# Kernel tuning notes

Hardware: AMD Instinct MI355X
Metric: run time of the kernel (lower is better)

## Reference

```python
import jax, jax.numpy as jnp
import numpy as np

# BCQLinear packed forward: weight[o, i] reconstructed from per-(out,group,bit)
# alpha scales and +/-1 binary codes via einsum('oib,oiab->oia'), then a plain
# out-channel-wise matmul (in_ch_wise=False) plus bias. beta is NOT used in the
# packed forward path of the original module.

B, S = 2, 1024          # token dims (m...)
O = 4096                 # out_features
G, A, NB = 32, 128, 3    # n_groups, group_size, n_bits; in_features = G*A = 4096


def setup_inputs() -> dict:
    key = jax.random.key(0)
    k1, k2, k3, k4 = jax.random.split(key, 4)
    x = jax.random.normal(k1, (B, S, G * A), dtype=jnp.float32)
    # binary codes are strictly +/-1 (Packer.unpack yields sign bits)
    b = jnp.sign(jax.random.normal(k2, (O, G, A, NB)))
    binary = jnp.where(b == 0, 1.0, b).astype(jnp.float32)
    # alpha scales are small positive magnitudes in practice
    alpha = jax.random.uniform(k3, (O, G, NB), dtype=jnp.float32,
                               minval=0.01, maxval=0.1)
    bias = 0.01 * jax.random.normal(k4, (O,), dtype=jnp.float32)
    return {"input": x, "binary": binary, "alpha": alpha, "bias": bias}


def reference(input, binary, alpha, bias):
    # dequantize: [O, G, A] -> [O, I]
    weight = jnp.einsum('oib,oiab->oia', alpha, binary).reshape(binary.shape[0], -1)
    # out-channel-wise matmul: m...i, oi -> m...o
    out = jnp.einsum('msi,oi->mso', input, weight) + bias
    return out
```

## Files before the change

### kernel.cpp

```cpp
#include <hip/hip_runtime.h>
#include <hip/hip_bf16.h>
#include <stdint.h>

typedef __bf16 bf16x8 __attribute__((ext_vector_type(8)));
typedef float  f32x4  __attribute__((ext_vector_type(4)));

static constexpr int Mdim = 2048;
static constexpr int Ndim = 4096;
static constexpr int Kdim = 4096;
static constexpr int DQ_BLOCKS = (Ndim * Kdim / 8) / 256;
static constexpr int CVT_BLOCKS = (Mdim * Kdim / 8) / 256;

__global__ __launch_bounds__(256)
void prep(const float* __restrict__ binary, const float* __restrict__ alpha,
          const float* __restrict__ x, __bf16* __restrict__ w,
          __bf16* __restrict__ xb) {
  const int b = blockIdx.x;
  if (b < DQ_BLOCKS) {
    long e = ((long)b * 256 + threadIdx.x) * 8;
    int o = (int)(e >> 12);
    int g = (int)((e & 4095) >> 7);
    const float* al = alpha + ((long)o * 32 + g) * 3;
    float a0 = al[0], a1 = al[1], a2 = al[2];
    const float4* q = (const float4*)(binary + e * 3);
    float4 q0 = q[0], q1 = q[1], q2 = q[2], q3 = q[3], q4 = q[4], q5 = q[5];
    bf16x8 wv;
    wv[0] = (__bf16)(a0 * q0.x + a1 * q0.y + a2 * q0.z);
    wv[1] = (__bf16)(a0 * q0.w + a1 * q1.x + a2 * q1.y);
    wv[2] = (__bf16)(a0 * q1.z + a1 * q1.w + a2 * q2.x);
    wv[3] = (__bf16)(a0 * q2.y + a1 * q2.z + a2 * q2.w);
    wv[4] = (__bf16)(a0 * q3.x + a1 * q3.y + a2 * q3.z);
    wv[5] = (__bf16)(a0 * q3.w + a1 * q4.x + a2 * q4.y);
    wv[6] = (__bf16)(a0 * q4.z + a1 * q4.w + a2 * q5.x);
    wv[7] = (__bf16)(a0 * q5.y + a1 * q5.z + a2 * q5.w);
    *(bf16x8*)(w + e) = wv;
  } else {
    long e = ((long)(b - DQ_BLOCKS) * 256 + threadIdx.x) * 8;
    float4 v0 = *(const float4*)(x + e);
    float4 v1 = *(const float4*)(x + e + 4);
    bf16x8 r;
    r[0] = (__bf16)v0.x; r[1] = (__bf16)v0.y; r[2] = (__bf16)v0.z; r[3] = (__bf16)v0.w;
    r[4] = (__bf16)v1.x; r[5] = (__bf16)v1.y; r[6] = (__bf16)v1.z; r[7] = (__bf16)v1.w;
    *(bf16x8*)(xb + e) = r;
  }
}

__global__ __launch_bounds__(256)
void reduce_add(const __bf16* __restrict__ p, const float* __restrict__ bias,
                float* __restrict__ out) {
  long e = ((long)blockIdx.x * 256 + threadIdx.x) * 8;
  bf16x8 a = *(const bf16x8*)(p + e);
  bf16x8 c = *(const bf16x8*)(p + (long)Mdim * Ndim + e);
  int col = (int)(e & (Ndim - 1));
  float4 bv0 = *(const float4*)(bias + col);
  float4 bv1 = *(const float4*)(bias + col + 4);
  float4 r0, r1;
  r0.x = (float)a[0] + (float)c[0] + bv0.x;
  r0.y = (float)a[1] + (float)c[1] + bv0.y;
  r0.z = (float)a[2] + (float)c[2] + bv0.z;
  r0.w = (float)a[3] + (float)c[3] + bv0.w;
  r1.x = (float)a[4] + (float)c[4] + bv1.x;
  r1.y = (float)a[5] + (float)c[5] + bv1.y;
  r1.z = (float)a[6] + (float)c[6] + bv1.z;
  r1.w = (float)a[7] + (float)c[7] + bv1.w;
  *(float4*)(out + e) = r0;
  *(float4*)(out + e + 4) = r1;
}

static constexpr int KSLICE = 2048;
static constexpr int NT = KSLICE / 64;
static constexpr int HB = 65536;

__device__ __forceinline__ void g2l16(const void* g, void* l) {
  __builtin_amdgcn_global_load_lds(
      (const __attribute__((address_space(1))) void*)g,
      (__attribute__((address_space(3))) void*)l, 16, 0, 0);
}

#define BAR()    __builtin_amdgcn_s_barrier()
#define LGKM0()  asm volatile("s_waitcnt lgkmcnt(0)" ::: "memory")
#define SCHED0() __builtin_amdgcn_sched_barrier(0)
#define GATE8()  asm volatile("s_waitcnt vmcnt(8)" ::: "memory")
#define GATE0()  asm volatile("s_waitcnt vmcnt(0)" ::: "memory")

#define STAGE_A1(t, bo) do { \
  g2l16(baseA +                 (long)(t) * 64, sm + (bo) +     0 + w * 1024); \
  g2l16(baseA + 128L * Kdim   + (long)(t) * 64, sm + (bo) + 16384 + w * 1024); \
} while (0)
#define STAGE_A2(t, bo) do { \
  g2l16(baseA +  64L * Kdim   + (long)(t) * 64, sm + (bo) +  8192 + w * 1024); \
  g2l16(baseA + 192L * Kdim   + (long)(t) * 64, sm + (bo) + 24576 + w * 1024); \
} while (0)
#define STAGE_B1(t, bo) do { \
  g2l16(baseB +                 (long)(t) * 64, sm + (bo) + 32768 + bq * 1024); \
  g2l16(baseB +   8L * Kdim   + (long)(t) * 64, sm + (bo) + 32768 + bq * 1024 + 1024); \
} while (0)
#define STAGE_B2(t, bo) do { \
  g2l16(baseB +  32L * Kdim   + (long)(t) * 64, sm + (bo) + 32768 + bq * 1024 + 4096); \
  g2l16(baseB +  40L * Kdim   + (long)(t) * 64, sm + (bo) + 32768 + bq * 1024 + 5120); \
} while (0)

#define LOAD_A4(dst, bo, m0_) do { \
  _Pragma("unroll") for (int m_ = 0; m_ < 4; ++m_) \
    _Pragma("unroll") for (int h_ = 0; h_ < 2; ++h_) \
      dst[m_][h_] = *(const bf16x8*)(sm + (bo) + aoffbase + ((m0_) + m_) * 2048 + swz[h_]); \
} while (0)
#define LOAD_B2(dst, bo, n0_) do { \
  _Pragma("unroll") for (int n_ = 0; n_ < 2; ++n_) \
    _Pragma("unroll") for (int h_ = 0; h_ < 2; ++h_) \
      dst[n_][h_] = *(const bf16x8*)(sm + (bo) + boffbase + ((n0_) + n_) * 2048 + swz[h_]); \
} while (0)

#define MMA8(fa_, fb_, m0_, n0_) do { \
  __builtin_amdgcn_s_setprio(1); \
  _Pragma("unroll") for (int m_ = 0; m_ < 4; ++m_) \
    _Pragma("unroll") for (int n_ = 0; n_ < 2; ++n_) { \
      acc[(m0_) + m_][(n0_) + n_] = __builtin_amdgcn_mfma_f32_16x16x32_bf16( \
          fa_[m_][0], fb_[n_][0], acc[(m0_) + m_][(n0_) + n_], 0, 0, 0); \
      acc[(m0_) + m_][(n0_) + n_] = __builtin_amdgcn_mfma_f32_16x16x32_bf16( \
          fa_[m_][1], fb_[n_][1], acc[(m0_) + m_][(n0_) + n_], 0, 0, 0); \
    } \
  __builtin_amdgcn_s_setprio(0); \
} while (0)

#define KTILE(t_, bo, PF_, LASTGATE) do { \
   \
  LOAD_A4(fa, bo, 0); LOAD_B2(fb01, bo, 0); \
  BAR(); LGKM0(); SCHED0(); \
  MMA8(fa, fb01, 0, 0); \
  BAR(); \
   \
  LOAD_B2(fb23, bo, 2); \
  if (PF_) { STAGE_A1((t_) + 2, bo); STAGE_B1((t_) + 2, bo); } \
  BAR(); LGKM0(); SCHED0(); \
  MMA8(fa, fb23, 0, 2); \
  BAR(); \
   \
  LOAD_A4(fa, bo, 4); \
  if (PF_) STAGE_B2((t_) + 2, bo); \
  BAR(); LGKM0(); SCHED0(); \
  MMA8(fa, fb01, 4, 0); \
  BAR(); \
   \
  if (PF_) { STAGE_A2((t_) + 2, bo); GATE8(); } else { LASTGATE; } \
  BAR(); \
  MMA8(fa, fb23, 4, 2); \
  BAR(); \
} while (0)

__global__ __launch_bounds__(512, 2)
void gemm256(const __bf16* __restrict__ A, const __bf16* __restrict__ Bw,
             __bf16* __restrict__ P) {
  __shared__ __align__(128) char sm[2 * HB];
  const int tid = threadIdx.x, lane = tid & 63, w = tid >> 6;
  const int wm = w >> 2, wn = w & 3;

  const int bid = blockIdx.x;
  const int logical = (bid & 7) * 32 + (bid >> 3);
  const int ks = logical >> 7;
  const int tile = logical & 127;
  const int tm = tile & 7, tn = tile >> 3;
  const int kbase = ks * KSLICE;

  __bf16* Pout = P + (long)ks * Mdim * Ndim;

  const int rlo = lane >> 3;
  const int gsw = (lane & 7) ^ rlo;
  const __bf16* baseA = A + (long)(tm * 256 + w * 8 + rlo) * Kdim + kbase + gsw * 8;
  const __bf16* baseB = Bw + (long)(tn * 256 + (w >> 1) * 64 + (w & 1) * 16 + rlo) * Kdim
                        + kbase + gsw * 8;
  const int bq = (w >> 1) * 8 + (w & 1) * 2;

  int swz[2];
#pragma unroll
  for (int h = 0; h < 2; ++h)
    swz[h] = (((h * 4 + (lane >> 4)) ^ (lane & 7)) << 4);
  const int aoffbase = (wm * 128 + (lane & 15)) * 128;
  const int boffbase = 32768 + (wn * 64 + (lane & 15)) * 128;

  f32x4 acc[8][4] = {};
  bf16x8 fa[4][2], fb01[2][2], fb23[2][2];

  STAGE_A1(0, 0);  STAGE_B1(0, 0);  STAGE_B2(0, 0);  STAGE_A2(0, 0);
  STAGE_A1(1, HB); STAGE_B1(1, HB); STAGE_B2(1, HB); STAGE_A2(1, HB);
  GATE8();
  BAR();

  for (int i = 0; i < NT / 2; ++i) {
    const int t0 = 2 * i, t1 = 2 * i + 1;
    const bool pf = (i < NT / 2 - 1);
    KTILE(t0, 0,  pf, GATE0());
    KTILE(t1, HB, pf, GATE0());
  }

  const int r4 = (lane >> 4) * 4;
  const int cl = lane & 15;
#pragma unroll
  for (int m = 0; m < 8; ++m)
#pragma unroll
    for (int n = 0; n < 4; ++n)
#pragma unroll
      for (int r = 0; r < 4; ++r) {
        int row = tm * 256 + wm * 128 + m * 16 + r4 + r;
        int col = tn * 256 + wn * 64 + n * 16 + cl;
        Pout[(long)row * Ndim + col] = (__bf16)acc[m][n][r];
      }
}

extern "C" void kernel_launch(void* const* d_in, const int* in_sizes, int n_in,
                              void* d_out, int out_size, void* d_ws, size_t ws_size,
                              hipStream_t stream) {
  const float* x      = (const float*)d_in[0];
  const float* binary = (const float*)d_in[1];
  const float* alpha  = (const float*)d_in[2];
  const float* bias   = (const float*)d_in[3];
  float* out = (float*)d_out;

  __bf16* wb = (__bf16*)d_ws;
  __bf16* xb = wb + (size_t)Ndim * Kdim;
  __bf16* pp = xb + (size_t)Mdim * Kdim;

  prep<<<dim3(DQ_BLOCKS + CVT_BLOCKS), 256, 0, stream>>>(binary, alpha, x, wb, xb);
  gemm256<<<dim3(256), 512, 0, stream>>>(xb, wb, pp);
  reduce_add<<<dim3(Mdim * Ndim / 8 / 256), 256, 0, stream>>>(pp, bias, out);
}
```

Before: 123.3 us.

## Fuse split-K reduction and bias into GEMM via per-tile atomic counters

Removes the separate reduce_add kernel. Each split-K block now writes its bf16 partial tile in a fragment-native layout and increments a per-tile atomic counter. The second block to arrive reads the other partial, adds it in registers, and writes the fp32 output plus bias through LDS so stores are coalesced. This saves a kernel launch and a full pass over the partial buffer, but adds atomics, cross-block memory-ordering requirements, and a serialized epilogue in the last-arriving block.

```diff
diff --git a/kernel.cpp b/kernel.cpp
--- a/kernel.cpp
+++ b/kernel.cpp
@@ -3,6 +3,7 @@
 #include <stdint.h>
 
 typedef __bf16 bf16x8 __attribute__((ext_vector_type(8)));
+typedef __bf16 bf16x4 __attribute__((ext_vector_type(4)));
 typedef float  f32x4  __attribute__((ext_vector_type(4)));
 
 static constexpr int Mdim = 2048;
@@ -14,10 +15,12 @@
 __global__ __launch_bounds__(256)
 void prep(const float* __restrict__ binary, const float* __restrict__ alpha,
           const float* __restrict__ x, __bf16* __restrict__ w,
-          __bf16* __restrict__ xb) {
+          __bf16* __restrict__ xb, int* __restrict__ flags) {
   const int b = blockIdx.x;
+  const int t = threadIdx.x;
+  if (b == 0 && t < 128) flags[t] = 0;
   if (b < DQ_BLOCKS) {
-    long e = ((long)b * 256 + threadIdx.x) * 8;
+    long e = ((long)b * 256 + t) * 8;
     int o = (int)(e >> 12);
     int g = (int)((e & 4095) >> 7);
     const float* al = alpha + ((long)o * 32 + g) * 3;
@@ -35,7 +38,7 @@
     wv[7] = (__bf16)(a0 * q5.y + a1 * q5.z + a2 * q5.w);
     *(bf16x8*)(w + e) = wv;
   } else {
-    long e = ((long)(b - DQ_BLOCKS) * 256 + threadIdx.x) * 8;
+    long e = ((long)(b - DQ_BLOCKS) * 256 + t) * 8;
     float4 v0 = *(const float4*)(x + e);
     float4 v1 = *(const float4*)(x + e + 4);
     bf16x8 r;
@@ -43,28 +46,6 @@
     r[4] = (__bf16)v1.x; r[5] = (__bf16)v1.y; r[6] = (__bf16)v1.z; r[7] = (__bf16)v1.w;
     *(bf16x8*)(xb + e) = r;
   }
-}
-
-__global__ __launch_bounds__(256)
-void reduce_add(const __bf16* __restrict__ p, const float* __restrict__ bias,
-                float* __restrict__ out) {
-  long e = ((long)blockIdx.x * 256 + threadIdx.x) * 8;
-  bf16x8 a = *(const bf16x8*)(p + e);
-  bf16x8 c = *(const bf16x8*)(p + (long)Mdim * Ndim + e);
-  int col = (int)(e & (Ndim - 1));
-  float4 bv0 = *(const float4*)(bias + col);
-  float4 bv1 = *(const float4*)(bias + col + 4);
-  float4 r0, r1;
-  r0.x = (float)a[0] + (float)c[0] + bv0.x;
-  r0.y = (float)a[1] + (float)c[1] + bv0.y;
-  r0.z = (float)a[2] + (float)c[2] + bv0.z;
-  r0.w = (float)a[3] + (float)c[3] + bv0.w;
-  r1.x = (float)a[4] + (float)c[4] + bv1.x;
-  r1.y = (float)a[5] + (float)c[5] + bv1.y;
-  r1.z = (float)a[6] + (float)c[6] + bv1.z;
-  r1.w = (float)a[7] + (float)c[7] + bv1.w;
-  *(float4*)(out + e) = r0;
-  *(float4*)(out + e + 4) = r1;
 }
 
 static constexpr int KSLICE = 2048;
@@ -150,8 +131,10 @@
 
 __global__ __launch_bounds__(512, 2)
 void gemm256(const __bf16* __restrict__ A, const __bf16* __restrict__ Bw,
-             __bf16* __restrict__ P) {
+             __bf16* __restrict__ PP, int* __restrict__ flags,
+             const float* __restrict__ bias, float* __restrict__ out) {
   __shared__ __align__(128) char sm[2 * HB];
+  __shared__ int role_sh;
   const int tid = threadIdx.x, lane = tid & 63, w = tid >> 6;
   const int wm = w >> 2, wn = w & 3;
 
@@ -162,8 +145,6 @@
   const int tm = tile & 7, tn = tile >> 3;
   const int kbase = ks * KSLICE;
 
-  __bf16* Pout = P + (long)ks * Mdim * Ndim;
-
   const int rlo = lane >> 3;
   const int gsw = (lane & 7) ^ rlo;
   const __bf16* baseA = A + (long)(tm * 256 + w * 8 + rlo) * Kdim + kbase + gsw * 8;
@@ -193,18 +174,67 @@
     KTILE(t1, HB, pf, GATE0());
   }
 
+  __bf16* pmy = PP + ((long)ks * 128 + tile) * 65536;
+  const __bf16* ppt = PP + ((long)(1 - ks) * 128 + tile) * 65536;
+#pragma unroll
+  for (int m = 0; m < 8; ++m)
+#pragma unroll
+    for (int n = 0; n < 4; ++n) {
+      bf16x4 pv;
+#pragma unroll
+      for (int r = 0; r < 4; ++r) pv[r] = (__bf16)acc[m][n][r];
+      *(bf16x4*)(pmy + (long)(m * 4 + n) * 2048 + tid * 4) = pv;
+    }
+  GATE0();
+  BAR();
+  if (tid == 0)
+    role_sh = (int)__hip_atomic_fetch_add(&flags[tile], 1, __ATOMIC_ACQ_REL,
+                                          __HIP_MEMORY_SCOPE_AGENT);
+  BAR();
+  if (role_sh == 0) return;
+
+#pragma unroll
+  for (int m = 0; m < 8; ++m)
+#pragma unroll
+    for (int n = 0; n < 4; ++n) {
+      unsigned long long u = __hip_atomic_load(
+          (const unsigned long long*)(ppt + (long)(m * 4 + n) * 2048 + tid * 4),
+          __ATOMIC_RELAXED, __HIP_MEMORY_SCOPE_AGENT);
+      bf16x4 pv = *(bf16x4*)&u;
+#pragma unroll
+      for (int r = 0; r < 4; ++r) acc[m][n][r] += (float)pv[r];
+    }
+
+  float* lf = (float*)sm;
   const int r4 = (lane >> 4) * 4;
   const int cl = lane & 15;
-#pragma unroll
-  for (int m = 0; m < 8; ++m)
-#pragma unroll
-    for (int n = 0; n < 4; ++n)
-#pragma unroll
-      for (int r = 0; r < 4; ++r) {
-        int row = tm * 256 + wm * 128 + m * 16 + r4 + r;
-        int col = tn * 256 + wn * 64 + n * 16 + cl;
-        Pout[(long)row * Ndim + col] = (__bf16)acc[m][n][r];
-      }
+  for (int c = 0; c < 4; ++c) {
+    if (wm == (c >> 1)) {
+      const int mlo = (c & 1) * 4;
+#pragma unroll
+      for (int mm = 0; mm < 4; ++mm)
+#pragma unroll
+        for (int n = 0; n < 4; ++n)
+#pragma unroll
+          for (int r = 0; r < 4; ++r) {
+            int rowc = mm * 16 + r4 + r;
+            int col = wn * 64 + n * 16 + cl;
+            lf[rowc * 260 + col] = acc[mlo + mm][n][r];
+          }
+    }
+    __syncthreads();
+#pragma unroll
+    for (int i = 0; i < 8; ++i) {
+      int idx = tid + i * 512;
+      int rowc = idx >> 6;
+      int c4 = idx & 63;
+      f32x4 v = *(const f32x4*)(lf + rowc * 260 + c4 * 4);
+      float4 bv = *(const float4*)(bias + tn * 256 + c4 * 4);
+      v[0] += bv.x; v[1] += bv.y; v[2] += bv.z; v[3] += bv.w;
+      *(f32x4*)(out + (long)(tm * 256 + c * 64 + rowc) * Ndim + tn * 256 + c4 * 4) = v;
+    }
+    __syncthreads();
+  }
 }
 
 extern "C" void kernel_launch(void* const* d_in, const int* in_sizes, int n_in,
@@ -219,8 +249,8 @@
   __bf16* wb = (__bf16*)d_ws;
   __bf16* xb = wb + (size_t)Ndim * Kdim;
   __bf16* pp = xb + (size_t)Mdim * Kdim;
-
-  prep<<<dim3(DQ_BLOCKS + CVT_BLOCKS), 256, 0, stream>>>(binary, alpha, x, wb, xb);
-  gemm256<<<dim3(256), 512, 0, stream>>>(xb, wb, pp);
-  reduce_add<<<dim3(Mdim * Ndim / 8 / 256), 256, 0, stream>>>(pp, bias, out);
-}
+  int*    fl = (int*)(pp + (size_t)256 * 65536);
+
+  prep<<<dim3(DQ_BLOCKS + CVT_BLOCKS), 256, 0, stream>>>(binary, alpha, x, wb, xb, fl);
+  gemm256<<<dim3(256), 512, 0, stream>>>(xb, wb, pp, fl, bias, out);
+}
```

Measured after the change: 127.4 us. 1.03x slower.
